# Kernel tuning notes

Measured on AMD Instinct MI355X. Metric: run time of the kernel, lower is better.

## Reference

```python
import jax, jax.numpy as jnp
import numpy as np

B, A, L, D, H = 8, 16, 80, 128, 6  # scenes, agents/scene, lanes/scene, feat dim, heads
LN_EPS = 1e-5


def _build_edges():
    hi_l, wi_l = [], []
    n_agt = B * A
    for b in range(B):
        ids = np.concatenate([np.arange(b * A, (b + 1) * A),
                              n_agt + np.arange(b * L, (b + 1) * L)])
        n = len(ids)
        hi_l.append(np.repeat(ids, n))  # 'd -> (d n)'
        wi_l.append(np.tile(ids, n))    # 'd -> (n d)'
    return (jnp.asarray(np.concatenate(hi_l), dtype=jnp.int32),
            jnp.asarray(np.concatenate(wi_l), dtype=jnp.int32))


def setup_inputs() -> dict:
    key = jax.random.key(0)
    ks = jax.random.split(key, 10)
    w = 0.05  # small init so exp(att) is well-behaved
    hi, wi = _build_edges()
    return {
        "agents": jax.random.normal(ks[0], (B * A, D), jnp.float32),
        "lanes": jax.random.normal(ks[1], (B * L, D), jnp.float32),
        "Wq": w * jax.random.normal(ks[2], (D, H * D), jnp.float32),
        "Wk": w * jax.random.normal(ks[3], (D, H * D), jnp.float32),
        "Wv": w * jax.random.normal(ks[4], (D, H * D), jnp.float32),
        "Wout1": w * jax.random.normal(ks[5], (H * D, D), jnp.float32),
        "Wout2": w * jax.random.normal(ks[6], (D, D), jnp.float32),
        "W1": w * jax.random.normal(ks[7], (D, D), jnp.float32),
        "ln_g": jnp.ones((D,), jnp.float32),
        "ln_b": jnp.zeros((D,), jnp.float32),
        "W2": w * jax.random.normal(ks[8], (D, D), jnp.float32),
        "hi": hi,
        "wi": wi,
    }


def _layernorm(x, g, b):
    mu = x.mean(-1, keepdims=True)
    var = ((x - mu) ** 2).mean(-1, keepdims=True)
    return (x - mu) * jax.lax.rsqrt(var + LN_EPS) * g + b


def reference(agents, lanes, Wq, Wk, Wv, Wout1, Wout2, W1, ln_g, ln_b, W2, hi, wi):
    nodes = jnp.concatenate([agents, lanes], axis=0)  # [N, D]
    N = nodes.shape[0]
    n_agt = agents.shape[0]
    scale = D ** -0.5

    src = nodes[hi]  # [E, D] (query side)
    dst = nodes[wi]  # [E, D] (key/value side)
    q = (src @ Wq).reshape(-1, H, D)
    k = (dst @ Wk).reshape(-1, H, D)
    v = jax.nn.relu(dst @ Wv).reshape(-1, H, D)

    att = jnp.einsum('ehd,ehd->eh', q, k) * scale          # [E, H]
    att = jnp.exp(att - att.max())                          # global-max-shifted exp (as in source)
    denom = jax.ops.segment_sum(att, hi, num_segments=N)    # [N, H]
    att = att / denom[hi]
    out = jax.ops.segment_sum(att[..., None] * v, hi, num_segments=N)  # [N, H, D]
    out = out.reshape(N, H * D)

    out = jax.nn.relu(out @ Wout1) @ Wout2                  # to_out
    h = _layernorm(nodes @ W1 + out, ln_g, ln_b)
    h = jax.nn.relu(h)
    h = h @ W2
    h = jax.nn.relu(h + nodes)                              # residual to pre-attention nodes
    return h[:n_agt]
```

## Files before the change

kernel.cpp:

```cpp
#include <hip/hip_runtime.h>
#include <math.h>

#define LN_EPS 1e-5f


__global__ __launch_bounds__(512) void k_attn(
    const float* __restrict__ agents, const float* __restrict__ lanes,
    const float* __restrict__ Wq, const float* __restrict__ Wk,
    const float* __restrict__ Wv, float* __restrict__ AO)
{
    __shared__ float smem[40384];
    float (*Ns)[132]  = (float (*)[132])(smem);
    float (*Wks)[132] = (float (*)[132])(smem + 12672);
    float (*Wvh)[68]  = (float (*)[68]) (smem + 29568);
    float (*Tt)[132]  = (float (*)[132])(smem + 38272);
    float (*Vh)[68]   = (float (*)[68]) (smem + 29568);
    float (*Qs)[132]  = (float (*)[132])(smem + 36096);
    float (*Sm)[20]   = (float (*)[20]) (smem + 12672);

    const int tid = threadIdx.x;
    const int b = blockIdx.x;
    const int s = b / 12, r12 = b % 12;
    const int h = r12 >> 1, half = r12 & 1;

    #pragma unroll
    for (int ii = 0; ii < 6; ++ii) {
        const int idx = tid + ii * 512;
        const int n = idx >> 5, c4 = idx & 31;
        const float* src = (n < 16) ? (agents + (size_t)(s * 16 + n) * 128)
                                    : (lanes + (size_t)(s * 80 + n - 16) * 128);
        *(float4*)&Ns[n][c4 * 4] = *(const float4*)(src + c4 * 4);
    }
    #pragma unroll
    for (int ii = 0; ii < 8; ++ii) {
        const int idx = tid + ii * 512;
        const int row = idx >> 5, c4 = idx & 31;
        *(float4*)&Wks[row][c4 * 4] =
            *(const float4*)(Wk + (size_t)row * 768 + h * 128 + c4 * 4);
    }
    #pragma unroll
    for (int ii = 0; ii < 4; ++ii) {
        const int idx = tid + ii * 512;
        const int row = idx >> 4, c4 = idx & 15;
        *(float4*)&Wvh[row][c4 * 4] =
            *(const float4*)(Wv + (size_t)row * 768 + h * 128 + half * 64 + c4 * 4);
    }
    __syncthreads();

    float4 vacc[6];
    float4 qacc0 = make_float4(0, 0, 0, 0), qacc1 = make_float4(0, 0, 0, 0);
    int vr = 0, vc4 = 0, qc = 0, qrg = 0;
    if (tid < 256) {
        vc4 = tid & 15; vr = tid >> 4;
        #pragma unroll
        for (int u = 0; u < 6; ++u) vacc[u] = make_float4(0, 0, 0, 0);
        #pragma unroll 2
        for (int k4 = 0; k4 < 32; ++k4) {
            float4 w[4];
            #pragma unroll
            for (int j = 0; j < 4; ++j)
                w[j] = *(const float4*)&Wvh[k4 * 4 + j][vc4 * 4];
            #pragma unroll
            for (int u = 0; u < 6; ++u) {
                const float4 nv = *(const float4*)&Ns[vr + 16 * u][k4 * 4];
                vacc[u].x += nv.x*w[0].x + nv.y*w[1].x + nv.z*w[2].x + nv.w*w[3].x;
                vacc[u].y += nv.x*w[0].y + nv.y*w[1].y + nv.z*w[2].y + nv.w*w[3].y;
                vacc[u].z += nv.x*w[0].z + nv.y*w[1].z + nv.z*w[2].z + nv.w*w[3].z;
                vacc[u].w += nv.x*w[0].w + nv.y*w[1].w + nv.z*w[2].w + nv.w*w[3].w;
            }
        }
    } else {
        const int t = tid - 256;
        qc = t & 31; qrg = t >> 5;
        const float* wp = Wq + (size_t)h * 128 + qc * 4;
        #pragma unroll 2
        for (int k4 = 0; k4 < 32; ++k4) {
            float4 w[4];
            #pragma unroll
            for (int j = 0; j < 4; ++j)
                w[j] = *(const float4*)(wp + (size_t)(k4 * 4 + j) * 768);
            const float4 n0 = *(const float4*)&Ns[2 * qrg][k4 * 4];
            const float4 n1 = *(const float4*)&Ns[2 * qrg + 1][k4 * 4];
            qacc0.x += n0.x*w[0].x + n0.y*w[1].x + n0.z*w[2].x + n0.w*w[3].x;
            qacc0.y += n0.x*w[0].y + n0.y*w[1].y + n0.z*w[2].y + n0.w*w[3].y;
            qacc0.z += n0.x*w[0].z + n0.y*w[1].z + n0.z*w[2].z + n0.w*w[3].z;
            qacc0.w += n0.x*w[0].w + n0.y*w[1].w + n0.z*w[2].w + n0.w*w[3].w;
            qacc1.x += n1.x*w[0].x + n1.y*w[1].x + n1.z*w[2].x + n1.w*w[3].x;
            qacc1.y += n1.x*w[0].y + n1.y*w[1].y + n1.z*w[2].y + n1.w*w[3].y;
            qacc1.z += n1.x*w[0].z + n1.y*w[1].z + n1.z*w[2].z + n1.w*w[3].z;
            qacc1.w += n1.x*w[0].w + n1.y*w[1].w + n1.z*w[2].w + n1.w*w[3].w;
        }
    }
    __syncthreads();

    if (tid < 256) {
        #pragma unroll
        for (int u = 0; u < 6; ++u) {
            float4 v = vacc[u];
            v.x = fmaxf(v.x, 0.f); v.y = fmaxf(v.y, 0.f);
            v.z = fmaxf(v.z, 0.f); v.w = fmaxf(v.w, 0.f);
            *(float4*)&Vh[vr + 16 * u][vc4 * 4] = v;
        }
    } else {
        *(float4*)&Qs[2 * qrg][qc * 4]     = qacc0;
        *(float4*)&Qs[2 * qrg + 1][qc * 4] = qacc1;
    }
    __syncthreads();

    const int r = tid >> 5, kc = tid & 31;
    if (tid < 128) {
        float acc[4][4] = {};
        #pragma unroll 4
        for (int c4 = 0; c4 < 32; ++c4) {
            float4 q[4], w[4];
            #pragma unroll
            for (int u = 0; u < 4; ++u)
                q[u] = *(const float4*)&Qs[r + 4 * u][c4 * 4];
            #pragma unroll
            for (int u = 0; u < 4; ++u)
                w[u] = *(const float4*)&Wks[kc + 32 * u][c4 * 4];
            #pragma unroll
            for (int ur = 0; ur < 4; ++ur)
                #pragma unroll
                for (int uk = 0; uk < 4; ++uk)
                    acc[ur][uk] += q[ur].x * w[uk].x + q[ur].y * w[uk].y
                                 + q[ur].z * w[uk].z + q[ur].w * w[uk].w;
        }
        #pragma unroll
        for (int ur = 0; ur < 4; ++ur)
            #pragma unroll
            for (int uk = 0; uk < 4; ++uk)
                Tt[r + 4 * ur][kc + 32 * uk] = acc[ur][uk];
    }
    __syncthreads();

    if (tid < 128) {
        const int jc = kc, iq = r;
        float s0[4] = {}, s1[4] = {}, s2[4] = {};
        #pragma unroll 4
        for (int kk = 0; kk < 32; ++kk) {
            float4 t[4];
            #pragma unroll
            for (int u = 0; u < 4; ++u)
                t[u] = *(const float4*)&Tt[iq + 4 * u][kk * 4];
            const float4 n0 = *(const float4*)&Ns[jc][kk * 4];
            const float4 n1 = *(const float4*)&Ns[jc + 32][kk * 4];
            const float4 n2 = *(const float4*)&Ns[jc + 64][kk * 4];
            #pragma unroll
            for (int u = 0; u < 4; ++u) {
                s0[u] += t[u].x*n0.x + t[u].y*n0.y + t[u].z*n0.z + t[u].w*n0.w;
                s1[u] += t[u].x*n1.x + t[u].y*n1.y + t[u].z*n1.z + t[u].w*n1.w;
                s2[u] += t[u].x*n2.x + t[u].y*n2.y + t[u].z*n2.z + t[u].w*n2.w;
            }
        }
        const float scale = 0.088388347648318447f;
        #pragma unroll
        for (int u = 0; u < 4; ++u) {
            const float a0 = s0[u] * scale, a1 = s1[u] * scale, a2 = s2[u] * scale;
            float m = fmaxf(fmaxf(a0, a1), a2);
            #pragma unroll
            for (int o = 16; o >= 1; o >>= 1) m = fmaxf(m, __shfl_xor(m, o, 32));
            const float e0 = __expf(a0 - m), e1 = __expf(a1 - m), e2 = __expf(a2 - m);
            float sum = e0 + e1 + e2;
            #pragma unroll
            for (int o = 16; o >= 1; o >>= 1) sum += __shfl_xor(sum, o, 32);
            const float inv = 1.0f / sum;
            const int i = iq + 4 * u;
            Sm[jc][i]      = e0 * inv;
            Sm[jc + 32][i] = e1 * inv;
            Sm[jc + 64][i] = e2 * inv;
        }
    }
    __syncthreads();

    if (tid < 64) {
        const int d4 = tid & 15, iq = tid >> 4;
        float4 acc[4] = {};
        #pragma unroll 2
        for (int j = 0; j < 96; ++j) {
            const float4 p = *(const float4*)&Sm[j][iq * 4];
            const float4 v = *(const float4*)&Vh[j][d4 * 4];
            const float pv[4] = {p.x, p.y, p.z, p.w};
            #pragma unroll
            for (int u = 0; u < 4; ++u) {
                acc[u].x += pv[u] * v.x; acc[u].y += pv[u] * v.y;
                acc[u].z += pv[u] * v.z; acc[u].w += pv[u] * v.w;
            }
        }
        #pragma unroll
        for (int u = 0; u < 4; ++u)
            *(float4*)(AO + (size_t)(s * 16 + iq * 4 + u) * 768 +
                       h * 128 + half * 64 + d4 * 4) = acc[u];
    }
}

__global__ __launch_bounds__(512) void k_tail(
    const float* __restrict__ AO, const float* __restrict__ agents,
    const float* __restrict__ Wout1, const float* __restrict__ Wout2,
    const float* __restrict__ W1, const float* __restrict__ ln_g,
    const float* __restrict__ ln_b, const float* __restrict__ W2,
    float* __restrict__ out)
{
    __shared__ float ao0[768], ao1[768];
    __shared__ float nr0[128], nr1[128];
    __shared__ float ps0[2048], ps1[2048];
    __shared__ float y10[128], y11[128];
    __shared__ float hb0[128], hb1[128];
    __shared__ float red[8];

    const int tid = threadIdx.x;
    const int a0 = blockIdx.x * 2, a1 = a0 + 1;

    if (tid < 192) {
        *(float4*)&ao0[tid * 4] = *(const float4*)(AO + (size_t)a0 * 768 + tid * 4);
    } else if (tid < 384) {
        const int t = tid - 192;
        *(float4*)&ao1[t * 4] = *(const float4*)(AO + (size_t)a1 * 768 + t * 4);
    } else if (tid < 416) {
        const int t = tid - 384;
        *(float4*)&nr0[t * 4] = *(const float4*)(agents + (size_t)a0 * 128 + t * 4);
    } else if (tid < 448) {
        const int t = tid - 416;
        *(float4*)&nr1[t * 4] = *(const float4*)(agents + (size_t)a1 * 128 + t * 4);
    }
    __syncthreads();

    const int d4 = tid & 31, g = tid >> 5;
    {
        float4 acc0 = make_float4(0, 0, 0, 0), acc1 = make_float4(0, 0, 0, 0);
        const int k0 = g * 48;
        #pragma unroll 8
        for (int k = 0; k < 48; ++k) {
            const float4 w = *(const float4*)(Wout1 + (size_t)(k0 + k) * 128 + d4 * 4);
            const float v0 = ao0[k0 + k], v1 = ao1[k0 + k];
            acc0.x += v0 * w.x; acc0.y += v0 * w.y; acc0.z += v0 * w.z; acc0.w += v0 * w.w;
            acc1.x += v1 * w.x; acc1.y += v1 * w.y; acc1.z += v1 * w.z; acc1.w += v1 * w.w;
        }
        *(float4*)&ps0[g * 128 + d4 * 4] = acc0;
        *(float4*)&ps1[g * 128 + d4 * 4] = acc1;
    }
    __syncthreads();
    if (tid < 128) {
        float u0 = 0.f, u1 = 0.f;
        #pragma unroll
        for (int gg = 0; gg < 16; ++gg) {
            u0 += ps0[gg * 128 + tid]; u1 += ps1[gg * 128 + tid];
        }
        y10[tid] = fmaxf(u0, 0.f); y11[tid] = fmaxf(u1, 0.f);
    }
    __syncthreads();
    {
        float4 acc0 = make_float4(0, 0, 0, 0), acc1 = make_float4(0, 0, 0, 0);
        const int k0 = g * 8;
        #pragma unroll
        for (int k = 0; k < 8; ++k) {
            const float4 w2v = *(const float4*)(Wout2 + (size_t)(k0 + k) * 128 + d4 * 4);
            const float4 w1v = *(const float4*)(W1 + (size_t)(k0 + k) * 128 + d4 * 4);
            const float v0 = y10[k0 + k], n0 = nr0[k0 + k];
            const float v1 = y11[k0 + k], n1 = nr1[k0 + k];
            acc0.x += v0 * w2v.x + n0 * w1v.x; acc0.y += v0 * w2v.y + n0 * w1v.y;
            acc0.z += v0 * w2v.z + n0 * w1v.z; acc0.w += v0 * w2v.w + n0 * w1v.w;
            acc1.x += v1 * w2v.x + n1 * w1v.x; acc1.y += v1 * w2v.y + n1 * w1v.y;
            acc1.z += v1 * w2v.z + n1 * w1v.z; acc1.w += v1 * w2v.w + n1 * w1v.w;
        }
        *(float4*)&ps0[g * 128 + d4 * 4] = acc0;
        *(float4*)&ps1[g * 128 + d4 * 4] = acc1;
    }
    __syncthreads();
    float t0 = 0.f, t1 = 0.f;
    if (tid < 128) {
        #pragma unroll
        for (int gg = 0; gg < 16; ++gg) {
            t0 += ps0[gg * 128 + tid]; t1 += ps1[gg * 128 + tid];
        }
    }
    float s10 = t0, s20 = t0 * t0, s11 = t1, s21 = t1 * t1;
    #pragma unroll
    for (int o = 32; o >= 1; o >>= 1) {
        s10 += __shfl_xor(s10, o); s20 += __shfl_xor(s20, o);
        s11 += __shfl_xor(s11, o); s21 += __shfl_xor(s21, o);
    }
    if (tid < 128 && (tid & 63) == 0) {
        const int wid = tid >> 6;
        red[wid * 4 + 0] = s10; red[wid * 4 + 1] = s20;
        red[wid * 4 + 2] = s11; red[wid * 4 + 3] = s21;
    }
    __syncthreads();
    if (tid < 128) {
        const float S10 = red[0] + red[4], S20 = red[1] + red[5];
        const float S11 = red[2] + red[6], S21 = red[3] + red[7];
        const float mu0 = S10 * (1.0f / 128.0f);
        const float var0 = S20 * (1.0f / 128.0f) - mu0 * mu0;
        const float mu1 = S11 * (1.0f / 128.0f);
        const float var1 = S21 * (1.0f / 128.0f) - mu1 * mu1;
        const float g_ = ln_g[tid], b_ = ln_b[tid];
        hb0[tid] = fmaxf((t0 - mu0) * rsqrtf(var0 + LN_EPS) * g_ + b_, 0.0f);
        hb1[tid] = fmaxf((t1 - mu1) * rsqrtf(var1 + LN_EPS) * g_ + b_, 0.0f);
    }
    __syncthreads();
    {
        float4 acc0 = make_float4(0, 0, 0, 0), acc1 = make_float4(0, 0, 0, 0);
        const int k0 = g * 8;
        #pragma unroll
        for (int k = 0; k < 8; ++k) {
            const float4 w = *(const float4*)(W2 + (size_t)(k0 + k) * 128 + d4 * 4);
            const float v0 = hb0[k0 + k], v1 = hb1[k0 + k];
            acc0.x += v0 * w.x; acc0.y += v0 * w.y; acc0.z += v0 * w.z; acc0.w += v0 * w.w;
            acc1.x += v1 * w.x; acc1.y += v1 * w.y; acc1.z += v1 * w.z; acc1.w += v1 * w.w;
        }
        *(float4*)&ps0[g * 128 + d4 * 4] = acc0;
        *(float4*)&ps1[g * 128 + d4 * 4] = acc1;
    }
    __syncthreads();
    if (tid < 128) {
        float o0 = nr0[tid], o1 = nr1[tid];
        #pragma unroll
        for (int gg = 0; gg < 16; ++gg) {
            o0 += ps0[gg * 128 + tid]; o1 += ps1[gg * 128 + tid];
        }
        out[(size_t)a0 * 128 + tid] = fmaxf(o0, 0.f);
        out[(size_t)a1 * 128 + tid] = fmaxf(o1, 0.f);
    }
}

extern "C" void kernel_launch(void* const* d_in, const int* in_sizes, int n_in,
                              void* d_out, int out_size, void* d_ws, size_t ws_size,
                              hipStream_t stream)
{
    const float* agents = (const float*)d_in[0];
    const float* lanes  = (const float*)d_in[1];
    const float* Wq     = (const float*)d_in[2];
    const float* Wk     = (const float*)d_in[3];
    const float* Wv     = (const float*)d_in[4];
    const float* Wout1  = (const float*)d_in[5];
    const float* Wout2  = (const float*)d_in[6];
    const float* W1     = (const float*)d_in[7];
    const float* ln_g   = (const float*)d_in[8];
    const float* ln_b   = (const float*)d_in[9];
    const float* W2     = (const float*)d_in[10];

    float* AO   = (float*)d_ws;
    float* outp = (float*)d_out;

    k_attn<<<96, 512, 0, stream>>>(agents, lanes, Wq, Wk, Wv, AO);
    k_tail<<<64, 512, 0, stream>>>(AO, agents, Wout1, Wout2, W1,
                                   ln_g, ln_b, W2, outp);
}
```

Baseline: 113.1 us.

## Split V projection into separate GEMM blocks and move PV product into tail kernel

Stage one now launches 240 blocks of 256 threads. 144 of them compute the full relu(nodes@Wv) as a tiled GEMM into a workspace buffer, and the other 96 compute Q, the folded Q·Wk^T and the softmax probabilities per scene, head and half of the agents, writing them to a second buffer. The attention-times-V product moves into the tail kernel, which reads the probabilities and the V rows from global memory before running the output MLP. The aim is more parallelism and shorter per-block critical paths in the first kernel. The cost is extra global round-trips for V and P, and Wk is now loaded in two pieces.

New measurement: 112.1 us. No clear change (-0.8%).

```diff
diff --git a/kernel.cpp b/kernel.cpp
--- a/kernel.cpp
+++ b/kernel.cpp
@@ -4,158 +4,211 @@
 #define LN_EPS 1e-5f
 
 
-__global__ __launch_bounds__(512) void k_attn(
+__global__ __launch_bounds__(256) void k_stage1(
     const float* __restrict__ agents, const float* __restrict__ lanes,
     const float* __restrict__ Wq, const float* __restrict__ Wk,
-    const float* __restrict__ Wv, float* __restrict__ AO)
+    const float* __restrict__ Wv, float* __restrict__ V,
+    float* __restrict__ P)
 {
-    __shared__ float smem[40384];
-    float (*Ns)[132]  = (float (*)[132])(smem);
-    float (*Wks)[132] = (float (*)[132])(smem + 12672);
-    float (*Wvh)[68]  = (float (*)[68]) (smem + 29568);
-    float (*Tt)[132]  = (float (*)[132])(smem + 38272);
-    float (*Vh)[68]   = (float (*)[68]) (smem + 29568);
-    float (*Qs)[132]  = (float (*)[132])(smem + 36096);
-    float (*Sm)[20]   = (float (*)[20]) (smem + 12672);
-
+    __shared__ float smem[40128];
     const int tid = threadIdx.x;
-    const int b = blockIdx.x;
-    const int s = b / 12, r12 = b % 12;
-    const int h = r12 >> 1, half = r12 & 1;
-
-    #pragma unroll
-    for (int ii = 0; ii < 6; ++ii) {
-        const int idx = tid + ii * 512;
-        const int n = idx >> 5, c4 = idx & 31;
-        const float* src = (n < 16) ? (agents + (size_t)(s * 16 + n) * 128)
-                                    : (lanes + (size_t)(s * 80 + n - 16) * 128);
-        *(float4*)&Ns[n][c4 * 4] = *(const float4*)(src + c4 * 4);
-    }
-    #pragma unroll
-    for (int ii = 0; ii < 8; ++ii) {
-        const int idx = tid + ii * 512;
-        const int row = idx >> 5, c4 = idx & 31;
-        *(float4*)&Wks[row][c4 * 4] =
-            *(const float4*)(Wk + (size_t)row * 768 + h * 128 + c4 * 4);
-    }
-    #pragma unroll
-    for (int ii = 0; ii < 4; ++ii) {
-        const int idx = tid + ii * 512;
-        const int row = idx >> 4, c4 = idx & 15;
-        *(float4*)&Wvh[row][c4 * 4] =
-            *(const float4*)(Wv + (size_t)row * 768 + h * 128 + half * 64 + c4 * 4);
-    }
-    __syncthreads();
-
-    float4 vacc[6];
-    float4 qacc0 = make_float4(0, 0, 0, 0), qacc1 = make_float4(0, 0, 0, 0);
-    int vr = 0, vc4 = 0, qc = 0, qrg = 0;
-    if (tid < 256) {
-        vc4 = tid & 15; vr = tid >> 4;
-        #pragma unroll
-        for (int u = 0; u < 6; ++u) vacc[u] = make_float4(0, 0, 0, 0);
-        #pragma unroll 2
-        for (int k4 = 0; k4 < 32; ++k4) {
-            float4 w[4];
-            #pragma unroll
-            for (int j = 0; j < 4; ++j)
-                w[j] = *(const float4*)&Wvh[k4 * 4 + j][vc4 * 4];
-            #pragma unroll
-            for (int u = 0; u < 6; ++u) {
-                const float4 nv = *(const float4*)&Ns[vr + 16 * u][k4 * 4];
-                vacc[u].x += nv.x*w[0].x + nv.y*w[1].x + nv.z*w[2].x + nv.w*w[3].x;
-                vacc[u].y += nv.x*w[0].y + nv.y*w[1].y + nv.z*w[2].y + nv.w*w[3].y;
-                vacc[u].z += nv.x*w[0].z + nv.y*w[1].z + nv.z*w[2].z + nv.w*w[3].z;
-                vacc[u].w += nv.x*w[0].w + nv.y*w[1].w + nv.z*w[2].w + nv.w*w[3].w;
-            }
-        }
-    } else {
-        const int t = tid - 256;
-        qc = t & 31; qrg = t >> 5;
-        const float* wp = Wq + (size_t)h * 128 + qc * 4;
-        #pragma unroll 2
-        for (int k4 = 0; k4 < 32; ++k4) {
-            float4 w[4];
-            #pragma unroll
-            for (int j = 0; j < 4; ++j)
-                w[j] = *(const float4*)(wp + (size_t)(k4 * 4 + j) * 768);
-            const float4 n0 = *(const float4*)&Ns[2 * qrg][k4 * 4];
-            const float4 n1 = *(const float4*)&Ns[2 * qrg + 1][k4 * 4];
-            qacc0.x += n0.x*w[0].x + n0.y*w[1].x + n0.z*w[2].x + n0.w*w[3].x;
-            qacc0.y += n0.x*w[0].y + n0.y*w[1].y + n0.z*w[2].y + n0.w*w[3].y;
-            qacc0.z += n0.x*w[0].z + n0.y*w[1].z + n0.z*w[2].z + n0.w*w[3].z;
-            qacc0.w += n0.x*w[0].w + n0.y*w[1].w + n0.z*w[2].w + n0.w*w[3].w;
-            qacc1.x += n1.x*w[0].x + n1.y*w[1].x + n1.z*w[2].x + n1.w*w[3].x;
-            qacc1.y += n1.x*w[0].y + n1.y*w[1].y + n1.z*w[2].y + n1.w*w[3].y;
-            qacc1.z += n1.x*w[0].z + n1.y*w[1].z + n1.z*w[2].z + n1.w*w[3].z;
-            qacc1.w += n1.x*w[0].w + n1.y*w[1].w + n1.z*w[2].w + n1.w*w[3].w;
-        }
-    }
-    __syncthreads();
-
-    if (tid < 256) {
-        #pragma unroll
-        for (int u = 0; u < 6; ++u) {
-            float4 v = vacc[u];
+    const int bid = blockIdx.x;
+
+    if (bid < 144) {
+        float (*As)[68] = (float (*)[68])(smem);
+        float (*Bs)[68] = (float (*)[68])(smem + 8704);
+        const int br = bid % 12, bc = bid / 12;
+        const int r0 = br * 64, wc0 = bc * 64;
+
+        {
+            const int row = tid >> 2, kv = tid & 3;
+            const int gr = r0 + row;
+            const float* src = (gr < 128) ? (agents + (size_t)gr * 128)
+                                          : (lanes + (size_t)(gr - 128) * 128);
+            #pragma unroll
+            for (int j = 0; j < 8; ++j) {
+                const int k0 = kv * 4 + j * 16;
+                const float4 a = *(const float4*)(src + k0);
+                As[k0 + 0][row] = a.x; As[k0 + 1][row] = a.y;
+                As[k0 + 2][row] = a.z; As[k0 + 3][row] = a.w;
+            }
+        }
+        {
+            const int kr = tid >> 4, c4 = tid & 15;
+            #pragma unroll
+            for (int i = 0; i < 8; ++i) {
+                const int k = kr + 16 * i;
+                *(float4*)&Bs[k][c4 * 4] =
+                    *(const float4*)(Wv + (size_t)k * 768 + wc0 + c4 * 4);
+            }
+        }
+        __syncthreads();
+        const int tx = tid & 15, ty = tid >> 4;
+        float acc[4][4] = {};
+        #pragma unroll 8
+        for (int k = 0; k < 128; ++k) {
+            const float4 a = *(const float4*)&As[k][ty * 4];
+            const float4 b = *(const float4*)&Bs[k][tx * 4];
+            const float av[4] = {a.x, a.y, a.z, a.w};
+            #pragma unroll
+            for (int i = 0; i < 4; ++i) {
+                acc[i][0] += av[i] * b.x; acc[i][1] += av[i] * b.y;
+                acc[i][2] += av[i] * b.z; acc[i][3] += av[i] * b.w;
+            }
+        }
+        #pragma unroll
+        for (int i = 0; i < 4; ++i) {
+            float4 v = make_float4(acc[i][0], acc[i][1], acc[i][2], acc[i][3]);
             v.x = fmaxf(v.x, 0.f); v.y = fmaxf(v.y, 0.f);
             v.z = fmaxf(v.z, 0.f); v.w = fmaxf(v.w, 0.f);
-            *(float4*)&Vh[vr + 16 * u][vc4 * 4] = v;
-        }
-    } else {
-        *(float4*)&Qs[2 * qrg][qc * 4]     = qacc0;
-        *(float4*)&Qs[2 * qrg + 1][qc * 4] = qacc1;
-    }
-    __syncthreads();
-
-    const int r = tid >> 5, kc = tid & 31;
-    if (tid < 128) {
-        float acc[4][4] = {};
+            *(float4*)(V + (size_t)(r0 + ty * 4 + i) * 768 + wc0 + tx * 4) = v;
+        }
+        return;
+    }
+
+    const int idx = bid - 144;
+    const int s = idx / 12, rr = idx % 12;
+    const int h = rr >> 1, rh = rr & 1;
+
+    float (*Ns)[132] = (float (*)[132])(smem);
+    float (*WA)[132] = (float (*)[132])(smem + 12672);
+    float (*WB)[132] = (float (*)[132])(smem + 29568);
+    float (*Qs)[132] = (float (*)[132])(smem + 38016);
+    float (*Tt)[132] = (float (*)[132])(smem + 39072);
+
+    #pragma unroll
+    for (int i = 0; i < 13; ++i) {
+        const int id2 = tid + i * 256;
+        if (id2 < 3168) {
+            const int n = id2 >> 5, c4 = id2 & 31;
+            const float* src = (n < 16) ? (agents + (size_t)(s * 16 + n) * 128)
+                                        : (lanes + (size_t)(s * 80 + n - 16) * 128);
+            *(float4*)&Ns[n][c4 * 4] = *(const float4*)(src + c4 * 4);
+        }
+    }
+    #pragma unroll
+    for (int i = 0; i < 16; ++i) {
+        const int id2 = tid + i * 256;
+        const int row = id2 >> 5, c4 = id2 & 31;
+        *(float4*)&WA[row][c4 * 4] =
+            *(const float4*)(Wq + (size_t)row * 768 + h * 128 + c4 * 4);
+    }
+    #pragma unroll
+    for (int i = 0; i < 8; ++i) {
+        const int id2 = tid + i * 256;
+        const int row = id2 >> 5, c4 = id2 & 31;
+        *(float4*)&WB[row][c4 * 4] =
+            *(const float4*)(Wk + (size_t)row * 768 + h * 128 + c4 * 4);
+    }
+    __syncthreads();
+
+    if (tid < 128) {
+        const int nc = tid & 31, rq = tid >> 5;
+        const int ra = rh * 8 + rq * 2;
+        float4 acc0 = make_float4(0, 0, 0, 0), acc1 = make_float4(0, 0, 0, 0);
         #pragma unroll 4
         for (int c4 = 0; c4 < 32; ++c4) {
-            float4 q[4], w[4];
-            #pragma unroll
-            for (int u = 0; u < 4; ++u)
-                q[u] = *(const float4*)&Qs[r + 4 * u][c4 * 4];
-            #pragma unroll
-            for (int u = 0; u < 4; ++u)
-                w[u] = *(const float4*)&Wks[kc + 32 * u][c4 * 4];
-            #pragma unroll
-            for (int ur = 0; ur < 4; ++ur)
-                #pragma unroll
-                for (int uk = 0; uk < 4; ++uk)
-                    acc[ur][uk] += q[ur].x * w[uk].x + q[ur].y * w[uk].y
-                                 + q[ur].z * w[uk].z + q[ur].w * w[uk].w;
-        }
-        #pragma unroll
-        for (int ur = 0; ur < 4; ++ur)
-            #pragma unroll
-            for (int uk = 0; uk < 4; ++uk)
-                Tt[r + 4 * ur][kc + 32 * uk] = acc[ur][uk];
-    }
-    __syncthreads();
-
-    if (tid < 128) {
-        const int jc = kc, iq = r;
-        float s0[4] = {}, s1[4] = {}, s2[4] = {};
+            float4 w[4];
+            #pragma unroll
+            for (int j = 0; j < 4; ++j)
+                w[j] = *(const float4*)&WA[c4 * 4 + j][nc * 4];
+            const float4 a0 = *(const float4*)&Ns[ra][c4 * 4];
+            const float4 a1 = *(const float4*)&Ns[ra + 1][c4 * 4];
+            acc0.x += a0.x*w[0].x + a0.y*w[1].x + a0.z*w[2].x + a0.w*w[3].x;
+            acc0.y += a0.x*w[0].y + a0.y*w[1].y + a0.z*w[2].y + a0.w*w[3].y;
+            acc0.z += a0.x*w[0].z + a0.y*w[1].z + a0.z*w[2].z + a0.w*w[3].z;
+            acc0.w += a0.x*w[0].w + a0.y*w[1].w + a0.z*w[2].w + a0.w*w[3].w;
+            acc1.x += a1.x*w[0].x + a1.y*w[1].x + a1.z*w[2].x + a1.w*w[3].x;
+            acc1.y += a1.x*w[0].y + a1.y*w[1].y + a1.z*w[2].y + a1.w*w[3].y;
+            acc1.z += a1.x*w[0].z + a1.y*w[1].z + a1.z*w[2].z + a1.w*w[3].z;
+            acc1.w += a1.x*w[0].w + a1.y*w[1].w + a1.z*w[2].w + a1.w*w[3].w;
+        }
+        *(float4*)&Qs[rq * 2][nc * 4]     = acc0;
+        *(float4*)&Qs[rq * 2 + 1][nc * 4] = acc1;
+    }
+    __syncthreads();
+
+    if (tid < 64) {
+        const int kc = tid & 15, rq = tid >> 4;
+        float acc[2][4] = {};
+        #pragma unroll 4
+        for (int c4 = 0; c4 < 32; ++c4) {
+            float4 w[4];
+            #pragma unroll
+            for (int j = 0; j < 4; ++j)
+                w[j] = *(const float4*)&WB[kc * 4 + j][c4 * 4];
+            const float4 a0 = *(const float4*)&Qs[rq * 2][c4 * 4];
+            const float4 a1 = *(const float4*)&Qs[rq * 2 + 1][c4 * 4];
+            #pragma unroll
+            for (int j = 0; j < 4; ++j) {
+                acc[0][j] += a0.x*w[j].x + a0.y*w[j].y + a0.z*w[j].z + a0.w*w[j].w;
+                acc[1][j] += a1.x*w[j].x + a1.y*w[j].y + a1.z*w[j].z + a1.w*w[j].w;
+            }
+        }
+        #pragma unroll
+        for (int u = 0; u < 2; ++u)
+            #pragma unroll
+            for (int j = 0; j < 4; ++j)
+                Tt[rq * 2 + u][kc * 4 + j] = acc[u][j];
+    } else {
+        const int t = tid - 64;
+        #pragma unroll
+        for (int i = 0; i < 11; ++i) {
+            const int id2 = t + i * 192;
+            if (id2 < 2048) {
+                const int row = id2 >> 5, c4 = id2 & 31;
+                *(float4*)&WA[row][c4 * 4] =
+                    *(const float4*)(Wk + (size_t)(64 + row) * 768 + h * 128 + c4 * 4);
+            }
+        }
+    }
+    __syncthreads();
+
+    if (tid < 64) {
+        const int kc = tid & 15, rq = tid >> 4;
+        float acc[2][4] = {};
+        #pragma unroll 4
+        for (int c4 = 0; c4 < 32; ++c4) {
+            float4 w[4];
+            #pragma unroll
+            for (int j = 0; j < 4; ++j)
+                w[j] = *(const float4*)&WA[kc * 4 + j][c4 * 4];
+            const float4 a0 = *(const float4*)&Qs[rq * 2][c4 * 4];
+            const float4 a1 = *(const float4*)&Qs[rq * 2 + 1][c4 * 4];
+            #pragma unroll
+            for (int j = 0; j < 4; ++j) {
+                acc[0][j] += a0.x*w[j].x + a0.y*w[j].y + a0.z*w[j].z + a0.w*w[j].w;
+                acc[1][j] += a1.x*w[j].x + a1.y*w[j].y + a1.z*w[j].z + a1.w*w[j].w;
+            }
+        }
+        #pragma unroll
+        for (int u = 0; u < 2; ++u)
+            #pragma unroll
+            for (int j = 0; j < 4; ++j)
+                Tt[rq * 2 + u][64 + kc * 4 + j] = acc[u][j];
+    }
+    __syncthreads();
+
+    if (tid < 128) {
+        const int jc = tid & 31, iq = tid >> 5;
+        float s0[2] = {}, s1[2] = {}, s2[2] = {};
         #pragma unroll 4
         for (int kk = 0; kk < 32; ++kk) {
-            float4 t[4];
-            #pragma unroll
-            for (int u = 0; u < 4; ++u)
-                t[u] = *(const float4*)&Tt[iq + 4 * u][kk * 4];
+            const float4 t0 = *(const float4*)&Tt[iq * 2][kk * 4];
+            const float4 t1 = *(const float4*)&Tt[iq * 2 + 1][kk * 4];
             const float4 n0 = *(const float4*)&Ns[jc][kk * 4];
             const float4 n1 = *(const float4*)&Ns[jc + 32][kk * 4];
             const float4 n2 = *(const float4*)&Ns[jc + 64][kk * 4];
-            #pragma unroll
-            for (int u = 0; u < 4; ++u) {
-                s0[u] += t[u].x*n0.x + t[u].y*n0.y + t[u].z*n0.z + t[u].w*n0.w;
-                s1[u] += t[u].x*n1.x + t[u].y*n1.y + t[u].z*n1.z + t[u].w*n1.w;
-                s2[u] += t[u].x*n2.x + t[u].y*n2.y + t[u].z*n2.z + t[u].w*n2.w;
-            }
+            s0[0] += t0.x*n0.x + t0.y*n0.y + t0.z*n0.z + t0.w*n0.w;
+            s1[0] += t0.x*n1.x + t0.y*n1.y + t0.z*n1.z + t0.w*n1.w;
+            s2[0] += t0.x*n2.x + t0.y*n2.y + t0.z*n2.z + t0.w*n2.w;
+            s0[1] += t1.x*n0.x + t1.y*n0.y + t1.z*n0.z + t1.w*n0.w;
+            s1[1] += t1.x*n1.x + t1.y*n1.y + t1.z*n1.z + t1.w*n1.w;
+            s2[1] += t1.x*n2.x + t1.y*n2.y + t1.z*n2.z + t1.w*n2.w;
         }
         const float scale = 0.088388347648318447f;
         #pragma unroll
-        for (int u = 0; u < 4; ++u) {
+        for (int u = 0; u < 2; ++u) {
             const float a0 = s0[u] * scale, a1 = s1[u] * scale, a2 = s2[u] * scale;
             float m = fmaxf(fmaxf(a0, a1), a2);
             #pragma unroll
@@ -165,63 +218,76 @@
             #pragma unroll
             for (int o = 16; o >= 1; o >>= 1) sum += __shfl_xor(sum, o, 32);
             const float inv = 1.0f / sum;
-            const int i = iq + 4 * u;
-            Sm[jc][i]      = e0 * inv;
-            Sm[jc + 32][i] = e1 * inv;
-            Sm[jc + 64][i] = e2 * inv;
-        }
-    }
-    __syncthreads();
-
-    if (tid < 64) {
-        const int d4 = tid & 15, iq = tid >> 4;
-        float4 acc[4] = {};
-        #pragma unroll 2
-        for (int j = 0; j < 96; ++j) {
-            const float4 p = *(const float4*)&Sm[j][iq * 4];
-            const float4 v = *(const float4*)&Vh[j][d4 * 4];
-            const float pv[4] = {p.x, p.y, p.z, p.w};
-            #pragma unroll
-            for (int u = 0; u < 4; ++u) {
-                acc[u].x += pv[u] * v.x; acc[u].y += pv[u] * v.y;
-                acc[u].z += pv[u] * v.z; acc[u].w += pv[u] * v.w;
-            }
-        }
-        #pragma unroll
-        for (int u = 0; u < 4; ++u)
-            *(float4*)(AO + (size_t)(s * 16 + iq * 4 + u) * 768 +
-                       h * 128 + half * 64 + d4 * 4) = acc[u];
+            const int i = rh * 8 + iq * 2 + u;
+            float* dst = P + ((size_t)((s * 6 + h) * 16 + i)) * 96;
+            dst[jc]      = e0 * inv;
+            dst[jc + 32] = e1 * inv;
+            dst[jc + 64] = e2 * inv;
+        }
     }
 }
 
-__global__ __launch_bounds__(512) void k_tail(
-    const float* __restrict__ AO, const float* __restrict__ agents,
-    const float* __restrict__ Wout1, const float* __restrict__ Wout2,
-    const float* __restrict__ W1, const float* __restrict__ ln_g,
-    const float* __restrict__ ln_b, const float* __restrict__ W2,
-    float* __restrict__ out)
+__global__ __launch_bounds__(512) void k_tail2(
+    const float* __restrict__ V, const float* __restrict__ P,
+    const float* __restrict__ agents, const float* __restrict__ Wout1,
+    const float* __restrict__ Wout2, const float* __restrict__ W1,
+    const float* __restrict__ ln_g, const float* __restrict__ ln_b,
+    const float* __restrict__ W2, float* __restrict__ out)
 {
+    __shared__ float SmL[12][96];
+    __shared__ float psv0[2][768], psv1[2][768];
     __shared__ float ao0[768], ao1[768];
     __shared__ float nr0[128], nr1[128];
     __shared__ float ps0[2048], ps1[2048];
-    __shared__ float y10[128], y11[128];
-    __shared__ float hb0[128], hb1[128];
+    __shared__ float y10[128], y11[128], hb0[128], hb1[128];
     __shared__ float red[8];
 
-    const int tid = threadIdx.x;
-    const int a0 = blockIdx.x * 2, a1 = a0 + 1;
-
+    const int tid = threadIdx.x, b = blockIdx.x;
+    const int s = b >> 3, pr = b & 7;
+    const int a0 = s * 16 + pr * 2, a1 = a0 + 1;
+
+    if (tid < 288) {
+        const int row = tid / 24, c4 = tid % 24;
+        const int h = row >> 1, aa = row & 1;
+        *(float4*)&SmL[row][c4 * 4] = *(const float4*)(
+            P + ((size_t)((s * 6 + h) * 16 + pr * 2 + aa)) * 96 + c4 * 4);
+    } else if (tid < 320) {
+        const int t = tid - 288;
+        *(float4*)&nr0[t * 4] = *(const float4*)(agents + (size_t)a0 * 128 + t * 4);
+    } else if (tid < 352) {
+        const int t = tid - 320;
+        *(float4*)&nr1[t * 4] = *(const float4*)(agents + (size_t)a1 * 128 + t * 4);
+    }
+    __syncthreads();
+
+    if (tid < 384) {
+        const int c4 = tid & 31, hh = (tid >> 5) % 6, jh = tid / 192;
+        const int col = hh * 128 + c4 * 4;
+        float4 acc0 = make_float4(0, 0, 0, 0), acc1 = make_float4(0, 0, 0, 0);
+        const int j0 = jh * 48;
+        #pragma unroll 4
+        for (int j = j0; j < j0 + 48; ++j) {
+            const int row = (j < 16) ? (s * 16 + j) : (128 + s * 80 + j - 16);
+            const float4 v = *(const float4*)(V + (size_t)row * 768 + col);
+            const float p0 = SmL[hh * 2][j], p1 = SmL[hh * 2 + 1][j];
+            acc0.x += p0 * v.x; acc0.y += p0 * v.y;
+            acc0.z += p0 * v.z; acc0.w += p0 * v.w;
+            acc1.x += p1 * v.x; acc1.y += p1 * v.y;
+            acc1.z += p1 * v.z; acc1.w += p1 * v.w;
+        }
+        *(float4*)&psv0[jh][col] = acc0;
+        *(float4*)&psv1[jh][col] = acc1;
+    }
+    __syncthreads();
     if (tid < 192) {
-        *(float4*)&ao0[tid * 4] = *(const float4*)(AO + (size_t)a0 * 768 + tid * 4);
-    } else if (tid < 384) {
-        const int t = tid - 192;
-        *(float4*)&ao1[t * 4] = *(const float4*)(AO + (size_t)a1 * 768 + t * 4);
-    } else if (tid < 416) {
-        const int t = tid - 384;
-        *(float4*)&nr0[t * 4] = *(const float4*)(agents + (size_t)a0 * 128 + t * 4);
-    } else if (tid < 448) {
-        const int t = tid - 416;
-        *(float4*)&nr1[t * 4] = *(const float4*)(agents + (size_t)a1 * 128 + t * 4);
+        const float4 x0 = *(const float4*)&psv0[0][tid * 4];
+        const float4 x1 = *(const float4*)&psv0[1][tid * 4];
+        const float4 y0 = *(const float4*)&psv1[0][tid * 4];
+        const float4 y1 = *(const float4*)&psv1[1][tid * 4];
+        *(float4*)&ao0[tid * 4] = make_float4(x0.x + x1.x, x0.y + x1.y,
+                                              x0.z + x1.z, x0.w + x1.w);
+        *(float4*)&ao1[tid * 4] = make_float4(y0.x + y1.x, y0.y + y1.y,
+                                              y0.z + y1.z, y0.w + y1.w);
     }
     __syncthreads();
 
@@ -339,10 +405,12 @@
     const float* ln_b   = (const float*)d_in[9];
     const float* W2     = (const float*)d_in[10];
 
-    float* AO   = (float*)d_ws;
+    float* ws = (float*)d_ws;
+    float* V    = ws;
+    float* P    = V + 768 * 768;
     float* outp = (float*)d_out;
 
-    k_attn<<<96, 512, 0, stream>>>(agents, lanes, Wq, Wk, Wv, AO);
-    k_tail<<<64, 512, 0, stream>>>(AO, agents, Wout1, Wout2, W1,
-                                   ln_g, ln_b, W2, outp);
+    k_stage1<<<240, 256, 0, stream>>>(agents, lanes, Wq, Wk, Wv, V, P);
+    k_tail2 <<<64, 512, 0, stream>>>(V, P, agents, Wout1, Wout2, W1,
+                                     ln_g, ln_b, W2, outp);
 }
```
